# Kernel tuning notes

Measured on AMD Instinct MI355X. Metric: run time of the kernel, lower is better.

Reference implementation:

```python
import jax, jax.numpy as jnp
import numpy as np
import math

B, S, HID = 2, 2048, 1024
NH = 16
HD = HID // NH          # 64
VD = HD // 2            # 32 value dim
TD = HD - VD            # 32 type dim
EPS = 1e-6


def setup_inputs() -> dict:
    key = jax.random.key(0)
    ks = jax.random.split(key, 12)
    std = 1.0 / math.sqrt(HID)
    xav = math.sqrt(6.0 / (TD + TD))
    return {
        "x": jax.random.normal(ks[0], (B, S, HID), dtype=jnp.float32),
        "q_w": jax.random.uniform(ks[1], (HID, HID), jnp.float32, -std, std),
        "q_b": jax.random.uniform(ks[2], (HID,), jnp.float32, -std, std),
        "k_w": jax.random.uniform(ks[3], (HID, HID), jnp.float32, -std, std),
        "k_b": jax.random.uniform(ks[4], (HID,), jnp.float32, -std, std),
        "v_w": jax.random.uniform(ks[5], (HID, HID), jnp.float32, -std, std),
        "v_b": jax.random.uniform(ks[6], (HID,), jnp.float32, -std, std),
        "out_w": jax.random.uniform(ks[7], (HID, HID), jnp.float32, -std, std),
        "out_b": jax.random.uniform(ks[8], (HID,), jnp.float32, -std, std),
        "type_bilinear": jax.random.uniform(ks[9], (NH, TD, TD), jnp.float32, -xav, xav),
        "type_bias": jnp.full((NH,), 2.0, dtype=jnp.float32),
        "mask": jnp.ones((B, S), dtype=jnp.int32),
    }


def reference(x, q_w, q_b, k_w, k_b, v_w, v_b, out_w, out_b, type_bilinear, type_bias, mask):
    # projections: [B,S,HID] -> [B,NH,S,HD]
    def proj(w, b):
        y = jnp.einsum("bsi,io->bso", x, w) + b
        return y.reshape(B, S, NH, HD).transpose(0, 2, 1, 3)

    q = proj(q_w, q_b)
    k = proj(k_w, k_b)
    v = proj(v_w, v_b)

    q_val, q_type = q[..., :VD], q[..., VD:]
    k_val, k_type = k[..., :VD], k[..., VD:]

    # standard value score: [B,NH,S,S]
    val_scores = jnp.einsum("bhqd,bhkd->bhqk", q_val, k_val) / math.sqrt(VD)

    # per-head bilinear type score: q_type @ W_h @ k_type^T + bias_h
    qt = jnp.einsum("bhqd,hde->bhqe", q_type, type_bilinear)
    type_scores = jnp.einsum("bhqe,bhke->bhqk", qt, k_type) + type_bias[None, :, None, None]
    type_unif = jax.nn.sigmoid(type_scores)

    scores = val_scores + jnp.log(type_unif + EPS)

    # mask: [B,S] -> broadcast over heads and query dim (keys masked)
    m = (mask[:, None, None, :] != 0)
    scores = jnp.where(m, scores, -jnp.inf)

    attn = jax.nn.softmax(scores, axis=-1)
    out = jnp.einsum("bhqk,bhkd->bhqd", attn, v)          # [B,NH,S,HD]
    out = out.transpose(0, 2, 1, 3).reshape(B, S, HID)
    return jnp.einsum("bsi,io->bso", out, out_w) + out_b
```

## Files before the change

kernel.cpp:

```cpp
#include <hip/hip_runtime.h>
#include <hip/hip_bf16.h>
#include <math.h>

typedef __attribute__((ext_vector_type(8))) short bf16x8;
typedef __attribute__((ext_vector_type(4))) float f32x4;
typedef __attribute__((ext_vector_type(4))) int   i32x4;

#define NHh 16
#define Sq  2048
#define HIDq 1024
#define HDq 64
#define LOG2E 1.4426950408889634f

#if __has_builtin(__builtin_amdgcn_exp2f)
#define EXP2F(x) __builtin_amdgcn_exp2f(x)
#else
#define EXP2F(x) exp2f(x)
#endif
#if __has_builtin(__builtin_amdgcn_rcpf)
#define RCPF(x) __builtin_amdgcn_rcpf(x)
#else
#define RCPF(x) (1.0f/(x))
#endif

__device__ __forceinline__ unsigned short f2bf(float f){
  union { float f; unsigned u; } v; v.f = f;
  unsigned r = v.u + 0x7fffu + ((v.u >> 16) & 1u);
  return (unsigned short)(r >> 16);
}
__device__ __forceinline__ float bf2f(unsigned short s){
  union { unsigned u; float f; } v; v.u = ((unsigned)s) << 16;
  return v.f;
}
__device__ __forceinline__ unsigned pk2bf(float lo, float hi){
  union { __hip_bfloat162 h; unsigned u; } w;
  w.h = __float22bfloat162_rn(make_float2(lo, hi));
  return w.u;
}

__device__ __forceinline__ void gload_lds16(const unsigned short* g, unsigned short* l){
  __builtin_amdgcn_global_load_lds(
      (const __attribute__((address_space(1))) unsigned int*)g,
      (__attribute__((address_space(3))) unsigned int*)l, 16, 0, 0);
}

__global__ __launch_bounds__(256) void convert_x(const float* __restrict__ in,
                                                 unsigned short* __restrict__ out, int n8,
                                                 const int* __restrict__ mask,
                                                 float* __restrict__ Mf){
  int bid = blockIdx.x;
  int nmain = gridDim.x - 2;
  if (bid >= nmain){
    int base = (bid - nmain)*2048 + threadIdx.x*8;
    #pragma unroll
    for (int j=0;j<8;j++) Mf[base+j] = mask[base+j] ? 0.f : -1e30f;
    return;
  }
  int i = bid*256 + threadIdx.x;
  if (i >= n8) return;
  const f32x4* p = (const f32x4*)(in + (size_t)i*8);
  f32x4 a = p[0], b = p[1];
  union { unsigned short us[8]; i32x4 v; } o;
  #pragma unroll
  for (int j=0;j<4;j++){ o.us[j] = f2bf(a[j]); o.us[4+j] = f2bf(b[j]); }
  *(i32x4*)(out + (size_t)i*8) = o.v;
}

__global__ __launch_bounds__(256) void transpose_w(const float* __restrict__ w0, const float* __restrict__ w1,
                                                   const float* __restrict__ w2, const float* __restrict__ w3,
                                                   unsigned short* __restrict__ wT){
  __shared__ float tile[32][33];
  int z = blockIdx.z;
  const float* w = (z==0)?w0:(z==1)?w1:(z==2)?w2:w3;
  unsigned short* dst = wT + (size_t)z*HIDq*HIDq;
  int tx = threadIdx.x, ty = threadIdx.y;
  int n0 = blockIdx.x*32, k0 = blockIdx.y*32;
  #pragma unroll
  for (int i=ty;i<32;i+=8) tile[i][tx] = w[(size_t)(k0+i)*HIDq + n0+tx];
  __syncthreads();
  #pragma unroll
  for (int i=ty;i<32;i+=8) dst[(size_t)(n0+i)*HIDq + k0+tx] = f2bf(tile[tx][i]);
}

__device__ __forceinline__ void gemm_core(const unsigned short* __restrict__ Ag,
                                          const unsigned short* __restrict__ Bg,
                                          unsigned short* As, unsigned short* Bs,
                                          int t, int wr, int wc, int lr, int g,
                                          f32x4 acc[4][4]){
  for (int k0=0; k0<HIDq; k0+=32){
    __syncthreads();
    #pragma unroll
    for (int i=0;i<2;i++){
      int flat = t + i*256;
      int row = flat>>2, kc = (flat&3)*8;
      *(i32x4*)&As[row*40+kc] = *(const i32x4*)(Ag + (size_t)row*HIDq + k0 + kc);
      *(i32x4*)&Bs[row*40+kc] = *(const i32x4*)(Bg + (size_t)row*HIDq + k0 + kc);
    }
    __syncthreads();
    bf16x8 af[4], bfv[4];
    #pragma unroll
    for (int m=0;m<4;m++) af[m]  = *(bf16x8*)&As[(wr+m*16+lr)*40 + g*8];
    #pragma unroll
    for (int n=0;n<4;n++) bfv[n] = *(bf16x8*)&Bs[(wc+n*16+lr)*40 + g*8];
    #pragma unroll
    for (int n=0;n<4;n++)
      #pragma unroll
      for (int m=0;m<4;m++)
        acc[n][m] = __builtin_amdgcn_mfma_f32_16x16x32_bf16(bfv[n], af[m], acc[n][m], 0,0,0);
  }
}

__global__ __launch_bounds__(256) void gemm_qkv(const unsigned short* __restrict__ xbf,
    const unsigned short* __restrict__ wT,
    const float* __restrict__ q_b, const float* __restrict__ k_b, const float* __restrict__ v_b,
    unsigned short* __restrict__ Qeff, unsigned short* __restrict__ Keff,
    unsigned short* __restrict__ Vt){
  __shared__ unsigned short As[128*40];
  __shared__ unsigned short Bs[128*40];
  const int t = threadIdx.x;
  const int wv = t>>6, lane = t&63, g = lane>>4, lr = lane&15;
  const int wr = (wv>>1)*64, wc = (wv&1)*64;
  f32x4 acc[4][4] = {};
  const int xb = blockIdx.x, yb = blockIdx.y;
  const float VS = 0.25501335f;

  if (xb < 16){
    const int row0 = yb*128, col0 = xb*128;
    gemm_core(xbf + (size_t)row0*HIDq, wT + (size_t)col0*HIDq, As, Bs, t, wr, wc, lr, g, acc);
    #pragma unroll
    for (int n=0;n<4;n++){
      #pragma unroll
      for (int m=0;m<4;m++){
        int row = row0 + wr + m*16 + lr;
        int b_ = row>>11, ss = row&2047;
        int colb = col0 + wc + n*16 + g*4;
        int seg = colb>>10, cw = colb&1023;
        int hh = cw>>6, d = cw&63;
        const float* bp = seg ? k_b : q_b;
        f32x4 bb = *(const f32x4*)&bp[cw];
        float sc = seg ? 1.0f : (d < 32 ? VS : -LOG2E);
        unsigned short* E = seg ? Keff : Qeff;
        float v0 = (acc[n][m][0]+bb[0])*sc, v1 = (acc[n][m][1]+bb[1])*sc;
        float v2 = (acc[n][m][2]+bb[2])*sc, v3 = (acc[n][m][3]+bb[3])*sc;
        union { unsigned u[2]; unsigned long long ll; } W;
        W.u[0] = pk2bf(v0,v1); W.u[1] = pk2bf(v2,v3);
        *(unsigned long long*)&E[(((size_t)b_*NHh+hh)*Sq+ss)*HDq + d] = W.ll;
      }
    }
  } else {
    const int row0 = (xb-16)*128, col0 = yb*128;
    gemm_core(wT + (size_t)2*HIDq*HIDq + (size_t)row0*HIDq, xbf + (size_t)col0*HIDq,
              As, Bs, t, wr, wc, lr, g, acc);
    #pragma unroll
    for (int n=0;n<4;n++){
      #pragma unroll
      for (int m=0;m<4;m++){
        int chan = row0 + wr + m*16 + lr;
        int hh = chan>>6, d = chan&63;
        float bv = v_b[chan];
        int colb = col0 + wc + n*16 + g*4;
        int b_ = colb>>11, ss = colb&2047;
        union { unsigned u[2]; unsigned long long ll; } W;
        W.u[0] = pk2bf(acc[n][m][0]+bv, acc[n][m][1]+bv);
        W.u[1] = pk2bf(acc[n][m][2]+bv, acc[n][m][3]+bv);
        *(unsigned long long*)&Vt[(((size_t)b_*NHh+hh)*HDq + d)*Sq + ss] = W.ll;
      }
    }
  }
}

__global__ __launch_bounds__(256) void gemm_out(const unsigned short* __restrict__ A,
                                                const unsigned short* __restrict__ Bt,
                                                const float* __restrict__ bias,
                                                float* __restrict__ C){
  __shared__ unsigned short As[128*40];
  __shared__ unsigned short Bs[128*40];
  const int t = threadIdx.x;
  const int wv = t>>6, lane = t&63, g = lane>>4, lr = lane&15;
  const int wr = (wv>>1)*64, wc = (wv&1)*64;
  const int row0 = blockIdx.y*128, col0 = blockIdx.x*128;
  f32x4 acc[4][4] = {};
  gemm_core(A + (size_t)row0*HIDq, Bt + (size_t)col0*HIDq, As, Bs, t, wr, wc, lr, g, acc);
  #pragma unroll
  for (int n=0;n<4;n++){
    #pragma unroll
    for (int m=0;m<4;m++){
      int row = row0 + wr + m*16 + lr;
      int colb = col0 + wc + n*16 + g*4;
      f32x4 bb = *(const f32x4*)&bias[colb];
      f32x4 o = acc[n][m] + bb;
      *(f32x4*)&C[(size_t)row*HIDq + colb] = o;
    }
  }
}

__global__ __launch_bounds__(512,2) void attn_kernel(
    const unsigned short* __restrict__ Qe, const unsigned short* __restrict__ Ke,
    const unsigned short* __restrict__ Vt, const float* __restrict__ Tb,
    const float* __restrict__ tbias, const float* __restrict__ Mf,
    unsigned short* __restrict__ Obuf)
{
  __shared__ __align__(16) unsigned char smem[81920];
  unsigned short* Ks0 = (unsigned short*)smem;
  unsigned short* Vs0 = (unsigned short*)(smem + 16384);
  unsigned short* Ks1 = (unsigned short*)(smem + 32768);
  unsigned short* Vs1 = (unsigned short*)(smem + 49152);
  unsigned short* Pl  = (unsigned short*)(smem + 65536);
  float* qls = (float*)(smem + 32768);
  unsigned short* qtls = Pl;

  const int t = threadIdx.x;
  const int dd = blockIdx.x;
  const int slot = dd>>3, xcd = dd&7;
  const int x = slot & 15;
  const int bh = ((slot>>4)<<3) | xcd;
  const int h = bh & 15, b = bh >> 4;
  const int q0 = x*128;
  const int wv = t>>6, lane = t&63, g = lane>>4, lr = lane&15;

  const unsigned short* Qb  = Qe + (((size_t)b*NHh+h)*Sq + q0)*HDq;
  const unsigned short* Kb  = Ke + ((size_t)b*NHh+h)*(size_t)Sq*HDq;
  const unsigned short* Vtb = Vt + ((size_t)b*NHh+h)*(size_t)HDq*Sq;
  const float* Mfb = Mf + (size_t)b*Sq;

  const int ch0 = (wv*2+0)*64 + lane, ch1 = (wv*2+1)*64 + lane;

  {
    int kr0 = ch0>>3, kc0 = ch0&7, kr1 = ch1>>3, kc1 = ch1&7;
    gload_lds16(Kb + (size_t)kr0*HDq + (kc0 ^ (kr0&7))*8, Ks0 + ch0*8);
    gload_lds16(Kb + (size_t)kr1*HDq + (kc1 ^ (kr1&7))*8, Ks0 + ch1*8);
    int vd0 = ch0>>4, vc0 = ch0&15, vd1 = ch1>>4, vc1 = ch1&15;
    gload_lds16(Vtb + (size_t)vd0*Sq + (vc0 ^ (vd0&15))*8, Vs0 + ch0*8);
    gload_lds16(Vtb + (size_t)vd1*Sq + (vc1 ^ (vd1&15))*8, Vs0 + ch1*8);
  }

  {
    int row = t>>2, c8 = (t&3)*8;
    bf16x8 v = *(const bf16x8*)(Qb + (size_t)row*HDq + 32 + c8);
    #pragma unroll
    for (int j=0;j<8;j++) qls[row*33 + c8 + j] = bf2f((unsigned short)v[j]);
  }
  __syncthreads();
  {
    int row = t&127, e0 = (t>>7)*8;
    const float* Th = Tb + (size_t)h*1024;
    float a[8] = {};
    #pragma unroll 4
    for (int d=0; d<32; d++){
      float qd = qls[row*33 + d];
      const f32x4* tp = (const f32x4*)(Th + d*32 + e0);
      f32x4 t0 = tp[0], t1 = tp[1];
      a[0]+=qd*t0[0]; a[1]+=qd*t0[1]; a[2]+=qd*t0[2]; a[3]+=qd*t0[3];
      a[4]+=qd*t1[0]; a[5]+=qd*t1[1]; a[6]+=qd*t1[2]; a[7]+=qd*t1[3];
    }
    __syncthreads();
    union { unsigned u[2]; unsigned long long ll; } W0, W1;
    W0.u[0]=pk2bf(a[0],a[1]); W0.u[1]=pk2bf(a[2],a[3]);
    W1.u[0]=pk2bf(a[4],a[5]); W1.u[1]=pk2bf(a[6],a[7]);
    *(unsigned long long*)&qtls[row*40 + e0]     = W0.ll;
    *(unsigned long long*)&qtls[row*40 + e0 + 4] = W1.ll;
  }
  bf16x8 qvf = *(const bf16x8*)(Qb + (size_t)(wv*16+lr)*HDq + g*8);
  __syncthreads();
  bf16x8 qtn = *(const bf16x8*)&qtls[(wv*16+lr)*40 + g*8];
  __syncthreads();

  const float tbn = -tbias[h]*LOG2E;
  const f32x4 tbc = {tbn,tbn,tbn,tbn};
  f32x4 oT[4] = {};
  f32x4 lsum = {0.f,0.f,0.f,0.f};
  unsigned short* Pw = &Pl[wv*1024 + lr*64];
  const int swp = (lr&7)*8;
  bf16x8 onesf;
  #pragma unroll
  for (int j=0;j<8;j++) onesf[j] = (short)0x3F80;

  unsigned short *Kc = Ks0, *Vc = Vs0, *Kn = Ks1, *Vn = Vs1;

  for (int kt=0; kt<Sq; kt+=128){
    f32x4 madd[2][4];
    #pragma unroll
    for (int kh2=0; kh2<2; kh2++)
      #pragma unroll
      for (int ks=0; ks<4; ks++)
        madd[kh2][ks] = *(const f32x4*)(Mfb + kt + kh2*64 + ks*16 + g*4);
    if (kt + 128 < Sq){
      int kt2 = kt + 128;
      int kr0 = ch0>>3, kc0 = ch0&7, kr1 = ch1>>3, kc1 = ch1&7;
      gload_lds16(Kb + (size_t)(kt2+kr0)*HDq + (kc0 ^ (kr0&7))*8, Kn + ch0*8);
      gload_lds16(Kb + (size_t)(kt2+kr1)*HDq + (kc1 ^ (kr1&7))*8, Kn + ch1*8);
      int vd0 = ch0>>4, vc0 = ch0&15, vd1 = ch1>>4, vc1 = ch1&15;
      gload_lds16(Vtb + (size_t)vd0*Sq + kt2 + (vc0 ^ (vd0&15))*8, Vn + ch0*8);
      gload_lds16(Vtb + (size_t)vd1*Sq + kt2 + (vc1 ^ (vd1&15))*8, Vn + ch1*8);
    }

    #pragma unroll
    for (int kh=0; kh<2; kh++){
      f32x4 sv[4], st[4];
      __builtin_amdgcn_s_setprio(1);
      #pragma unroll
      for (int ks=0; ks<4; ks++){
        int krow = kh*64 + ks*16 + lr;
        const unsigned short* kb = &Kc[krow*64];
        int sw = (krow&7)*8;
        bf16x8 kf0 = *(const bf16x8*)(kb + ((g*8) ^ sw));
        bf16x8 kf1 = *(const bf16x8*)(kb + ((32 + g*8) ^ sw));
        sv[ks] = __builtin_amdgcn_mfma_f32_16x16x32_bf16(kf0, qvf, madd[kh][ks], 0,0,0);
        st[ks] = __builtin_amdgcn_mfma_f32_16x16x32_bf16(kf1, qtn, tbc, 0,0,0);
      }
      __builtin_amdgcn_s_setprio(0);
      #pragma unroll
      for (int ks=0; ks<4; ks++){
        float p0 = EXP2F(sv[ks][0]) * RCPF(1.f + EXP2F(st[ks][0]));
        float p1 = EXP2F(sv[ks][1]) * RCPF(1.f + EXP2F(st[ks][1]));
        float p2 = EXP2F(sv[ks][2]) * RCPF(1.f + EXP2F(st[ks][2]));
        float p3 = EXP2F(sv[ks][3]) * RCPF(1.f + EXP2F(st[ks][3]));
        union { unsigned u[2]; unsigned long long ll; } W;
        W.u[0] = pk2bf(p0,p1); W.u[1] = pk2bf(p2,p3);
        *(unsigned long long*)(Pw + ((ks*16 + g*4) ^ swp)) = W.ll;
      }
      #pragma unroll
      for (int ks2=0; ks2<2; ks2++){
        bf16x8 pf = *(const bf16x8*)(Pw + ((ks2*32 + g*8) ^ swp));
        __builtin_amdgcn_s_setprio(1);
        lsum = __builtin_amdgcn_mfma_f32_16x16x32_bf16(onesf, pf, lsum, 0,0,0);
        #pragma unroll
        for (int db=0; db<4; db++){
          int vrow = db*16 + lr;
          bf16x8 vf = *(const bf16x8*)(&Vc[vrow*128] + ((kh*64 + ks2*32 + g*8) ^ ((vrow&15)*8)));
          oT[db] = __builtin_amdgcn_mfma_f32_16x16x32_bf16(vf, pf, oT[db], 0,0,0);
        }
        __builtin_amdgcn_s_setprio(0);
      }
    }
    __syncthreads();
    unsigned short* tp;
    tp = Kc; Kc = Kn; Kn = tp;
    tp = Vc; Vc = Vn; Vn = tp;
  }

  float linv = (lsum[0] > 0.f) ? RCPF(lsum[0]) : 0.f;
  int srow = q0 + wv*16 + lr;
  unsigned short* Ob = Obuf + ((size_t)b*Sq + srow)*HIDq + h*HDq;
  #pragma unroll
  for (int db=0; db<4; db++){
    union { unsigned u[2]; unsigned long long ll; } W;
    W.u[0] = pk2bf(oT[db][0]*linv, oT[db][1]*linv);
    W.u[1] = pk2bf(oT[db][2]*linv, oT[db][3]*linv);
    *(unsigned long long*)(Ob + db*16 + g*4) = W.ll;
  }
}

extern "C" void kernel_launch(void* const* d_in, const int* in_sizes, int n_in,
                              void* d_out, int out_size, void* d_ws, size_t ws_size,
                              hipStream_t stream) {
  const float* x     = (const float*)d_in[0];
  const float* q_w   = (const float*)d_in[1];
  const float* q_b   = (const float*)d_in[2];
  const float* k_w   = (const float*)d_in[3];
  const float* k_b   = (const float*)d_in[4];
  const float* v_w   = (const float*)d_in[5];
  const float* v_b   = (const float*)d_in[6];
  const float* out_w = (const float*)d_in[7];
  const float* out_b = (const float*)d_in[8];
  const float* Tb    = (const float*)d_in[9];
  const float* tbias = (const float*)d_in[10];
  const int*   mask  = (const int*)d_in[11];

  const size_t MROWS = 4096;
  unsigned short* xbf  = (unsigned short*)d_ws;
  unsigned short* wT   = xbf  + MROWS*HIDq;
  unsigned short* Qeff = wT   + (size_t)4*HIDq*HIDq;
  unsigned short* Keff = Qeff + MROWS*HIDq;
  unsigned short* Vt   = Keff + MROWS*HIDq;
  unsigned short* Obuf = Vt   + MROWS*HIDq;
  float*          Mf   = (float*)(Obuf + MROWS*HIDq);

  int n8 = (int)(MROWS*HIDq/8);
  convert_x<<<dim3(n8/256 + 2), dim3(256), 0, stream>>>(x, xbf, n8, mask, Mf);
  transpose_w<<<dim3(32,32,4), dim3(32,8), 0, stream>>>(q_w, k_w, v_w, out_w, wT);

  gemm_qkv<<<dim3(24,32), dim3(256), 0, stream>>>(xbf, wT, q_b, k_b, v_b, Qeff, Keff, Vt);

  attn_kernel<<<dim3(512), dim3(512), 0, stream>>>(Qeff, Keff, Vt, Tb, tbias, Mf, Obuf);

  gemm_out<<<dim3(8,32), dim3(256), 0, stream>>>(Obuf, wT + (size_t)3*HIDq*HIDq, out_b, (float*)d_out);
}
```

Baseline: 170.9 us.

## Use direct global-to-LDS loads with XOR swizzle and K-tile of 64 in GEMMs

```diff
diff --git a/kernel.cpp b/kernel.cpp
--- a/kernel.cpp
+++ b/kernel.cpp
@@ -82,31 +82,41 @@
   for (int i=ty;i<32;i+=8) dst[(size_t)(n0+i)*HIDq + k0+tx] = f2bf(tile[tx][i]);
 }
 
-__device__ __forceinline__ void gemm_core(const unsigned short* __restrict__ Ag,
-                                          const unsigned short* __restrict__ Bg,
-                                          unsigned short* As, unsigned short* Bs,
-                                          int t, int wr, int wc, int lr, int g,
-                                          f32x4 acc[4][4]){
-  for (int k0=0; k0<HIDq; k0+=32){
+__device__ __forceinline__ void gemm_core_gl(const unsigned short* __restrict__ Ag,
+                                             const unsigned short* __restrict__ Bg,
+                                             unsigned short* As, unsigned short* Bs,
+                                             int t, int wv, int lane, int wr, int wc, int lr, int g,
+                                             f32x4 acc[4][4]){
+  for (int k0=0; k0<HIDq; k0+=64){
     __syncthreads();
     #pragma unroll
-    for (int i=0;i<2;i++){
-      int flat = t + i*256;
-      int row = flat>>2, kc = (flat&3)*8;
-      *(i32x4*)&As[row*40+kc] = *(const i32x4*)(Ag + (size_t)row*HIDq + k0 + kc);
-      *(i32x4*)&Bs[row*40+kc] = *(const i32x4*)(Bg + (size_t)row*HIDq + k0 + kc);
+    for (int j=0;j<4;j++){
+      int flat = (j*4+wv)*64 + lane;
+      int row = flat>>3, c = flat&7;
+      int srcc = (c ^ (row&7))*8;
+      gload_lds16(Ag + (size_t)row*HIDq + k0 + srcc, &As[flat*8]);
+      gload_lds16(Bg + (size_t)row*HIDq + k0 + srcc, &Bs[flat*8]);
     }
     __syncthreads();
-    bf16x8 af[4], bfv[4];
-    #pragma unroll
-    for (int m=0;m<4;m++) af[m]  = *(bf16x8*)&As[(wr+m*16+lr)*40 + g*8];
-    #pragma unroll
-    for (int n=0;n<4;n++) bfv[n] = *(bf16x8*)&Bs[(wc+n*16+lr)*40 + g*8];
-    #pragma unroll
-    for (int n=0;n<4;n++)
-      #pragma unroll
-      for (int m=0;m<4;m++)
-        acc[n][m] = __builtin_amdgcn_mfma_f32_16x16x32_bf16(bfv[n], af[m], acc[n][m], 0,0,0);
+    #pragma unroll
+    for (int ks=0; ks<2; ks++){
+      bf16x8 af[4], bfv[4];
+      #pragma unroll
+      for (int m=0;m<4;m++){
+        int rr = wr + m*16 + lr;
+        af[m]  = *(bf16x8*)&As[rr*64 + (((ks*4+g) ^ (rr&7))*8)];
+      }
+      #pragma unroll
+      for (int n=0;n<4;n++){
+        int rr = wc + n*16 + lr;
+        bfv[n] = *(bf16x8*)&Bs[rr*64 + (((ks*4+g) ^ (rr&7))*8)];
+      }
+      #pragma unroll
+      for (int n=0;n<4;n++)
+        #pragma unroll
+        for (int m=0;m<4;m++)
+          acc[n][m] = __builtin_amdgcn_mfma_f32_16x16x32_bf16(bfv[n], af[m], acc[n][m], 0,0,0);
+    }
   }
 }
 
@@ -115,8 +125,8 @@
     const float* __restrict__ q_b, const float* __restrict__ k_b, const float* __restrict__ v_b,
     unsigned short* __restrict__ Qeff, unsigned short* __restrict__ Keff,
     unsigned short* __restrict__ Vt){
-  __shared__ unsigned short As[128*40];
-  __shared__ unsigned short Bs[128*40];
+  __shared__ unsigned short As[128*64];
+  __shared__ unsigned short Bs[128*64];
   const int t = threadIdx.x;
   const int wv = t>>6, lane = t&63, g = lane>>4, lr = lane&15;
   const int wr = (wv>>1)*64, wc = (wv&1)*64;
@@ -126,7 +136,7 @@
 
   if (xb < 16){
     const int row0 = yb*128, col0 = xb*128;
-    gemm_core(xbf + (size_t)row0*HIDq, wT + (size_t)col0*HIDq, As, Bs, t, wr, wc, lr, g, acc);
+    gemm_core_gl(xbf + (size_t)row0*HIDq, wT + (size_t)col0*HIDq, As, Bs, t, wv, lane, wr, wc, lr, g, acc);
     #pragma unroll
     for (int n=0;n<4;n++){
       #pragma unroll
@@ -149,8 +159,8 @@
     }
   } else {
     const int row0 = (xb-16)*128, col0 = yb*128;
-    gemm_core(wT + (size_t)2*HIDq*HIDq + (size_t)row0*HIDq, xbf + (size_t)col0*HIDq,
-              As, Bs, t, wr, wc, lr, g, acc);
+    gemm_core_gl(wT + (size_t)2*HIDq*HIDq + (size_t)row0*HIDq, xbf + (size_t)col0*HIDq,
+                 As, Bs, t, wv, lane, wr, wc, lr, g, acc);
     #pragma unroll
     for (int n=0;n<4;n++){
       #pragma unroll
@@ -173,14 +183,14 @@
                                                 const unsigned short* __restrict__ Bt,
                                                 const float* __restrict__ bias,
                                                 float* __restrict__ C){
-  __shared__ unsigned short As[128*40];
-  __shared__ unsigned short Bs[128*40];
+  __shared__ unsigned short As[128*64];
+  __shared__ unsigned short Bs[128*64];
   const int t = threadIdx.x;
   const int wv = t>>6, lane = t&63, g = lane>>4, lr = lane&15;
   const int wr = (wv>>1)*64, wc = (wv&1)*64;
   const int row0 = blockIdx.y*128, col0 = blockIdx.x*128;
   f32x4 acc[4][4] = {};
-  gemm_core(A + (size_t)row0*HIDq, Bt + (size_t)col0*HIDq, As, Bs, t, wr, wc, lr, g, acc);
+  gemm_core_gl(A + (size_t)row0*HIDq, Bt + (size_t)col0*HIDq, As, Bs, t, wv, lane, wr, wc, lr, g, acc);
   #pragma unroll
   for (int n=0;n<4;n++){
     #pragma unroll
```

Result: faster. 159.6 us (-6.6%).
